# Kernel tuning notes

Measured on AMD Instinct MI355X. Metric: run time of the kernel, lower is better.

Reference implementation:

```python
import jax, jax.numpy as jnp
import numpy as np

D, K, HID, NBLK, N = 128, 256, 256, 2, 4096

def setup_inputs() -> dict:
    key = jax.random.key(0)
    ks = jax.random.split(key, 12)
    inp = {
        'x': jax.random.normal(ks[0], (N, D), jnp.float32),
        'x_hat': jax.random.normal(ks[1], (N, D), jnp.float32),
        'base_codebook': jax.random.normal(ks[2], (K, D), jnp.float32) * 0.1,
        # concat_proj: Linear(2D -> D), torch weight layout (out, in)
        'Wp': jax.random.normal(ks[3], (D, 2 * D), jnp.float32) / np.sqrt(2 * D),
        'bp': jnp.zeros((D,), jnp.float32),
        # residual blocks stacked over NBLK: Linear(D->HID), ReLU, Linear(HID->D)
        'W1': jax.random.normal(ks[4], (NBLK, HID, D), jnp.float32) / np.sqrt(D),
        'b1': jnp.zeros((NBLK, HID), jnp.float32),
        'W2': jax.random.normal(ks[5], (NBLK, D, HID), jnp.float32) / np.sqrt(HID),
        'b2': jnp.zeros((NBLK, D), jnp.float32),
    }
    return inp

def _forward(x, x_hat, base_codebook, Wp, bp, W1, b1, W2, b2):
    # concat_proj([x_hat, cbar]) decomposed: avoids materializing (N,K,2D)
    x_part = x_hat @ Wp[:, :D].T                      # (N, D)
    c_part = base_codebook @ Wp[:, D:].T + bp          # (K, D)
    C = x_part[:, None, :] + c_part[None, :, :]        # (N, K, D)
    for i in range(NBLK):
        h = jax.nn.relu(jnp.einsum('nkd,hd->nkh', C, W1[i]) + b1[i])
        C = C + jnp.einsum('nkh,dh->nkd', h, W2[i]) + b2[i]
    r = x - x_hat                                      # (N, D)
    dists = jnp.sum((r[:, None, :] - C) ** 2, axis=-1) # (N, K)
    codes = jnp.argmin(dists, axis=-1)                 # (N,)
    c_sel = jnp.take_along_axis(C, codes[:, None, None], axis=1)[:, 0, :]
    x_hat_new = x_hat + c_sel
    return codes, x_hat_new, r, c_sel

def reference(x, x_hat, base_codebook, Wp, bp, W1, b1, W2, b2):
    return _forward(x, x_hat, base_codebook, Wp, bp, W1, b1, W2, b2)
```

## Files before the change

kernel.cpp:

```cpp
#include <hip/hip_runtime.h>


#define QD    128
#define QK    256
#define QHID  256
#define QNBLK 2
#define QN    4096

typedef _Float16 f16;
typedef _Float16 f16x8  __attribute__((ext_vector_type(8)));
typedef float    f32x16 __attribute__((ext_vector_type(16)));
typedef unsigned u32x2  __attribute__((ext_vector_type(2)));

#define WS_CPART 0
#define WS_W1H   131072
#define WS_W1L   262144
#define WS_W2H   393216
#define WS_W2L   524288

#define L_WBUF  0
#define L_B1    65536
#define L_B2    67584
#define L_REDD  68608
#define L_REDI  69632
#define L_XP    70656
#define L_XH    71168
#define L_RS    71680
#define L_CSEL  72192
#define L_TOTAL 72704

static __device__ __forceinline__ f32x16 MF32(f16x8 a, f16x8 b, f32x16 c) {
    return __builtin_amdgcn_mfma_f32_32x32x16_f16(a, b, c, 0, 0, 0);
}
static __device__ __forceinline__ unsigned pkrtz(float a, float b) {
    return __builtin_bit_cast(unsigned, __builtin_amdgcn_cvt_pkrtz(a, b));
}
static __device__ __forceinline__ float f32lo(unsigned p) {
    return (float)__builtin_bit_cast(f16, (unsigned short)(p & 0xffffu));
}
static __device__ __forceinline__ float f32hi(unsigned p) {
    return (float)__builtin_bit_cast(f16, (unsigned short)(p >> 16));
}
static __device__ __forceinline__ u32x2 plswap(unsigned a, unsigned b) {
    return __builtin_amdgcn_permlane32_swap(a, b, false, false);
}
static __device__ __forceinline__ void gload_lds16(const void* g, void* l) {
    __builtin_amdgcn_global_load_lds(
        (const __attribute__((address_space(1))) unsigned*)g,
        (__attribute__((address_space(3))) unsigned*)l, 16, 0, 0);
}

template<int RB>
static __device__ __forceinline__ void split_frags(f32x16 a, f16x8& fh, f16x8& fl) {
    unsigned P0 = pkrtz(a[RB + 0], a[RB + 1]);
    unsigned P1 = pkrtz(a[RB + 2], a[RB + 3]);
    unsigned Q0 = pkrtz(a[RB + 4], a[RB + 5]);
    unsigned Q1 = pkrtz(a[RB + 6], a[RB + 7]);
    unsigned L0 = pkrtz(a[RB + 0] - f32lo(P0), a[RB + 1] - f32hi(P0));
    unsigned L1 = pkrtz(a[RB + 2] - f32lo(P1), a[RB + 3] - f32hi(P1));
    unsigned L2 = pkrtz(a[RB + 4] - f32lo(Q0), a[RB + 5] - f32hi(Q0));
    unsigned L3 = pkrtz(a[RB + 6] - f32lo(Q1), a[RB + 7] - f32hi(Q1));
    u32x2 s0 = plswap(P0, Q0);
    u32x2 s1 = plswap(P1, Q1);
    u32x2 t0 = plswap(L0, L2);
    u32x2 t1 = plswap(L1, L3);
    uint4 hw = make_uint4(s0.x, s1.x, s0.y, s1.y);
    uint4 lw = make_uint4(t0.x, t1.x, t0.y, t1.y);
    fh = __builtin_bit_cast(f16x8, hw);
    fl = __builtin_bit_cast(f16x8, lw);
}

__global__ __launch_bounds__(128) void qinco_prep(
    const float* __restrict__ cb, const float* __restrict__ Wp,
    const float* __restrict__ bp, const float* __restrict__ W1,
    const float* __restrict__ W2, char* __restrict__ ws) {
    const int blk = blockIdx.x;
    const int t = threadIdx.x;
    __shared__ float row[QD];

    if (blk < 256) {
        float* cpart = (float*)(ws + WS_CPART);
        row[t] = cb[blk * QD + t];
        __syncthreads();
        float acc = bp[t];
        const float* wr = Wp + (size_t)t * (2 * QD) + QD;
        #pragma unroll 8
        for (int e = 0; e < QD; ++e) acc = fmaf(row[e], wr[e], acc);
        cpart[blk * QD + t] = acc;
    } else if (blk < 384) {
        if (t < 64) {
            const int cid = blk - 256;
            const int b = cid >> 6, hc = (cid >> 3) & 7, kc = cid & 7;
            const int m = t & 31, g = t >> 5;
            f16* w1h = (f16*)(ws + WS_W1H);
            f16* w1l = (f16*)(ws + WS_W1L);
            #pragma unroll
            for (int j = 0; j < 8; ++j) {
                float wv = W1[((size_t)b * QHID + hc * 32 + m) * QD + kc * 16 + g * 8 + j];
                f16 hi = (f16)wv;
                size_t idx = ((size_t)cid * 64 + t) * 8 + j;
                w1h[idx] = hi;
                w1l[idx] = (f16)(wv - (float)hi);
            }
        }
    } else {
        if (t < 64) {
            const int e = blk - 384;
            const int b = e >> 6, hc = (e >> 3) & 7, dt = (e >> 1) & 3, kch = e & 1;
            const int m = t & 31, g = t >> 5;
            f16* w2h = (f16*)(ws + WS_W2H);
            f16* w2l = (f16*)(ws + WS_W2L);
            #pragma unroll
            for (int j = 0; j < 8; ++j) {
                float wv = W2[((size_t)b * QD + dt * 32 + m) * QHID + hc * 32 + kch * 16 + g * 8 + j];
                f16 hi = (f16)wv;
                size_t idx = ((size_t)e * 64 + t) * 8 + j;
                w2h[idx] = hi;
                w2l[idx] = (f16)(wv - (float)hi);
            }
        }
    }
}

__global__ __launch_bounds__(512, 2) void qinco_main(
    const float* __restrict__ x, const float* __restrict__ xh,
    const float* __restrict__ Wp,
    const float* __restrict__ b1g, const float* __restrict__ b2g,
    const char* __restrict__ ws, float* __restrict__ out) {

    extern __shared__ char smem[];
    const int n = blockIdx.x;
    const int t = threadIdx.x;
    const int w = t >> 6;
    const int l = t & 63;
    const int c32 = l & 31;
    const int g = l >> 5;
    const int baserow = w * 32;
    const int plane = w >> 1;
    const int jbase = (w & 1) * 4;

    float* b1_s  = (float*)(smem + L_B1);
    float* b2_s  = (float*)(smem + L_B2);
    float* red_d = (float*)(smem + L_REDD);
    int*   red_i = (int*)(smem + L_REDI);
    float* xp_s  = (float*)(smem + L_XP);
    float* xh_s  = (float*)(smem + L_XH);
    float* r_s   = (float*)(smem + L_RS);
    float* csel  = (float*)(smem + L_CSEL);

    const float* cpart = (const float*)(ws + WS_CPART);

    b1_s[t] = b1g[t];
    if (t < 2 * QD) b2_s[t] = b2g[t];
    if (t < QD) {
        float xv  = x[(size_t)n * QD + t];
        float xhv = xh[(size_t)n * QD + t];
        xh_s[t] = xhv;
        r_s[t]  = xv - xhv;
    }
    __syncthreads();

    if (t < QD) {
        const float4* wr = (const float4*)(Wp + (size_t)t * (2 * QD));
        const float4* xv = (const float4*)xh_s;
        float acc = 0.f;
        #pragma unroll
        for (int j = 0; j < QD / 4; ++j) {
            float4 a = wr[j], bv = xv[j];
            acc = fmaf(a.x, bv.x, acc);
            acc = fmaf(a.y, bv.y, acc);
            acc = fmaf(a.z, bv.z, acc);
            acc = fmaf(a.w, bv.w, acc);
        }
        xp_s[t] = acc;
    }
    __syncthreads();

    f32x16 Cacc[4];
    {
        const float* cprow = cpart + (size_t)(baserow + c32) * QD;
        #pragma unroll
        for (int dt = 0; dt < 4; ++dt)
            #pragma unroll
            for (int rq = 0; rq < 4; ++rq) {
                const int off = dt * 32 + 8 * rq + 4 * g;
                float4 cp  = *(const float4*)(cprow + off);
                float4 xp4 = *(const float4*)(xp_s + off);
                Cacc[dt][rq * 4 + 0] = cp.x + xp4.x;
                Cacc[dt][rq * 4 + 1] = cp.y + xp4.y;
                Cacc[dt][rq * 4 + 2] = cp.z + xp4.z;
                Cacc[dt][rq * 4 + 3] = cp.w + xp4.w;
            }
    }

    {
        const char* s0 = ws + (size_t)(plane + 1) * 131072 + (size_t)jbase * 1024
                       + (size_t)l * 16;
        char* d0 = smem + L_WBUF + (size_t)(plane * 8 + jbase) * 1024;
        #pragma unroll
        for (int ii = 0; ii < 4; ++ii)
            gload_lds16(s0 + (size_t)ii * 1024, d0 + (size_t)ii * 1024);
    }

    f16x8 cfh[8], cfl[8];

    #pragma unroll 1
    for (int iter = 0; iter < 16; ++iter) {
        const int cur = iter & 1;
        const int b = iter >> 3;
        const int hc = iter & 7;

        asm volatile("s_waitcnt vmcnt(0)" ::: "memory");
        __syncthreads();

        if (iter < 15) {
            const int it2 = iter + 1;
            const int bb = it2 >> 3, hh = it2 & 7;
            const char* s0 = ws + (size_t)(plane + 1) * 131072 + (size_t)bb * 65536
                           + (size_t)(hh * 8 + jbase) * 1024 + (size_t)l * 16;
            char* d0 = smem + L_WBUF + (size_t)(cur ^ 1) * 32768
                     + (size_t)(plane * 8 + jbase) * 1024;
            #pragma unroll
            for (int ii = 0; ii < 4; ++ii)
                gload_lds16(s0 + (size_t)ii * 1024, d0 + (size_t)ii * 1024);
        }

        if (hc == 0) {
            #pragma unroll
            for (int dt = 0; dt < 4; ++dt) {
                split_frags<0>(Cacc[dt], cfh[dt * 2 + 0], cfl[dt * 2 + 0]);
                split_frags<8>(Cacc[dt], cfh[dt * 2 + 1], cfl[dt * 2 + 1]);
            }
        }

        const char* wb = (const char*)smem + L_WBUF + (size_t)cur * 32768
                       + (size_t)l * 16;

        f32x16 Ha, Hb, Hc;
        #pragma unroll
        for (int rq = 0; rq < 4; ++rq) {
            float4 bv = *(const float4*)(b1_s + b * QHID + hc * 32 + 8 * rq + 4 * g);
            Ha[rq * 4 + 0] = bv.x;
            Ha[rq * 4 + 1] = bv.y;
            Ha[rq * 4 + 2] = bv.z;
            Ha[rq * 4 + 3] = bv.w;
        }
        #pragma unroll
        for (int r = 0; r < 16; ++r) { Hb[r] = 0.f; Hc[r] = 0.f; }

        __builtin_amdgcn_s_setprio(1);
        #pragma unroll
        for (int kc = 0; kc < 8; ++kc) {
            f16x8 wh = *(const f16x8*)(wb + kc * 1024);
            f16x8 wl = *(const f16x8*)(wb + 8192 + kc * 1024);
            Ha = MF32(wh, cfh[kc], Ha);
            Hb = MF32(wl, cfh[kc], Hb);
            Hc = MF32(wh, cfl[kc], Hc);
        }
        __builtin_amdgcn_s_setprio(0);

        f32x16 H;
        #pragma unroll
        for (int r = 0; r < 16; ++r)
            H[r] = fmaxf(Ha[r] + Hb[r] + Hc[r], 0.f);

        f16x8 hfh0, hfl0, hfh1, hfl1;
        split_frags<0>(H, hfh0, hfl0);
        split_frags<8>(H, hfh1, hfl1);

        __builtin_amdgcn_s_setprio(1);
        #pragma unroll
        for (int dt = 0; dt < 4; ++dt) {
            const char* q2h = wb + 16384 + (size_t)(dt * 2) * 1024;
            const char* q2l = wb + 24576 + (size_t)(dt * 2) * 1024;
            f16x8 w2h0 = *(const f16x8*)(q2h);
            f16x8 w2l0 = *(const f16x8*)(q2l);
            f16x8 w2h1 = *(const f16x8*)(q2h + 1024);
            f16x8 w2l1 = *(const f16x8*)(q2l + 1024);
            Cacc[dt] = MF32(w2h0, hfh0, Cacc[dt]);
            Cacc[dt] = MF32(w2l0, hfh0, Cacc[dt]);
            Cacc[dt] = MF32(w2h0, hfl0, Cacc[dt]);
            Cacc[dt] = MF32(w2h1, hfh1, Cacc[dt]);
            Cacc[dt] = MF32(w2l1, hfh1, Cacc[dt]);
            Cacc[dt] = MF32(w2h1, hfl1, Cacc[dt]);
        }
        __builtin_amdgcn_s_setprio(0);

        if (hc == 7) {
            #pragma unroll
            for (int dt = 0; dt < 4; ++dt)
                #pragma unroll
                for (int rq = 0; rq < 4; ++rq) {
                    float4 bv = *(const float4*)(b2_s + b * QD + dt * 32 + 8 * rq + 4 * g);
                    Cacc[dt][rq * 4 + 0] += bv.x;
                    Cacc[dt][rq * 4 + 1] += bv.y;
                    Cacc[dt][rq * 4 + 2] += bv.z;
                    Cacc[dt][rq * 4 + 3] += bv.w;
                }
        }
    }

    float pa = 0.f, pb = 0.f, pc = 0.f, pdm = 0.f;
    #pragma unroll
    for (int dt = 0; dt < 4; ++dt)
        #pragma unroll
        for (int rq = 0; rq < 4; ++rq) {
            float4 rr = *(const float4*)(r_s + dt * 32 + 8 * rq + 4 * g);
            float t0 = rr.x - Cacc[dt][rq * 4 + 0];
            float t1 = rr.y - Cacc[dt][rq * 4 + 1];
            float t2 = rr.z - Cacc[dt][rq * 4 + 2];
            float t3 = rr.w - Cacc[dt][rq * 4 + 3];
            pa = fmaf(t0, t0, pa);
            pb = fmaf(t1, t1, pb);
            pc = fmaf(t2, t2, pc);
            pdm = fmaf(t3, t3, pdm);
        }
    float pd = (pa + pb) + (pc + pdm);
    pd += __shfl_xor(pd, 32);
    if (l < 32) {
        red_d[baserow + l] = pd;
        red_i[baserow + l] = baserow + l;
    }
    __syncthreads();

    for (int off = 128; off > 0; off >>= 1) {
        if (t < off) {
            float d2 = red_d[t + off]; int i2 = red_i[t + off];
            float d1 = red_d[t];       int i1 = red_i[t];
            if (d2 < d1 || (d2 == d1 && i2 < i1)) { red_d[t] = d2; red_i[t] = i2; }
        }
        __syncthreads();
    }
    const int code = red_i[0];

    if (w == (code >> 5) && c32 == (code & 31)) {
        #pragma unroll
        for (int dt = 0; dt < 4; ++dt)
            #pragma unroll
            for (int rq = 0; rq < 4; ++rq)
                *(float4*)(csel + dt * 32 + 8 * rq + 4 * g) =
                    make_float4(Cacc[dt][rq * 4 + 0], Cacc[dt][rq * 4 + 1],
                                Cacc[dt][rq * 4 + 2], Cacc[dt][rq * 4 + 3]);
    }
    __syncthreads();

    if (t == 0) out[n] = (float)code;
    if (t < QD) {
        float cs  = csel[t];
        out[QN + (size_t)n * QD + t]                       = xh_s[t] + cs;
        out[QN + (size_t)QN * QD + (size_t)n * QD + t]     = r_s[t];
        out[QN + 2 * (size_t)QN * QD + (size_t)n * QD + t] = cs;
    }
}

extern "C" void kernel_launch(void* const* d_in, const int* in_sizes, int n_in,
                              void* d_out, int out_size, void* d_ws, size_t ws_size,
                              hipStream_t stream) {
    const float* x   = (const float*)d_in[0];
    const float* xh  = (const float*)d_in[1];
    const float* cb  = (const float*)d_in[2];
    const float* Wp  = (const float*)d_in[3];
    const float* bp  = (const float*)d_in[4];
    const float* W1  = (const float*)d_in[5];
    const float* b1  = (const float*)d_in[6];
    const float* W2  = (const float*)d_in[7];
    const float* b2  = (const float*)d_in[8];
    float* out = (float*)d_out;

    qinco_prep<<<512, 128, 0, stream>>>(cb, Wp, bp, W1, W2, (char*)d_ws);

    (void)hipFuncSetAttribute((const void*)qinco_main,
                              hipFuncAttributeMaxDynamicSharedMemorySize, L_TOTAL);
    qinco_main<<<QN, 512, L_TOTAL, stream>>>(x, xh, Wp, b1, b2,
                                             (const char*)d_ws, out);
}
```

Baseline: 716.0 us.

## Triple-buffer weight tiles in LDS with two-ahead prefetch and software-pipelined MFMA

```diff
diff --git a/kernel.cpp b/kernel.cpp
--- a/kernel.cpp
+++ b/kernel.cpp
@@ -19,15 +19,15 @@
 #define WS_W2L   524288
 
 #define L_WBUF  0
-#define L_B1    65536
-#define L_B2    67584
-#define L_REDD  68608
-#define L_REDI  69632
-#define L_XP    70656
-#define L_XH    71168
-#define L_RS    71680
-#define L_CSEL  72192
-#define L_TOTAL 72704
+#define L_B1    98304
+#define L_B2    100352
+#define L_REDD  101376
+#define L_REDI  102400
+#define L_XP    103424
+#define L_XH    103936
+#define L_RS    104448
+#define L_CSEL  104960
+#define L_TOTAL 105472
 
 static __device__ __forceinline__ f32x16 MF32(f16x8 a, f16x8 b, f32x16 c) {
     return __builtin_amdgcn_mfma_f32_32x32x16_f16(a, b, c, 0, 0, 0);
@@ -193,10 +193,12 @@
             }
     }
 
-    {
-        const char* s0 = ws + (size_t)(plane + 1) * 131072 + (size_t)jbase * 1024
-                       + (size_t)l * 16;
-        char* d0 = smem + L_WBUF + (size_t)(plane * 8 + jbase) * 1024;
+    #pragma unroll
+    for (int tt = 0; tt < 2; ++tt) {
+        const char* s0 = ws + (size_t)(plane + 1) * 131072
+                       + (size_t)(tt * 8 + jbase) * 1024 + (size_t)l * 16;
+        char* d0 = smem + L_WBUF + (size_t)tt * 32768
+                 + (size_t)(plane * 8 + jbase) * 1024;
         #pragma unroll
         for (int ii = 0; ii < 4; ++ii)
             gload_lds16(s0 + (size_t)ii * 1024, d0 + (size_t)ii * 1024);
@@ -206,24 +208,24 @@
 
     #pragma unroll 1
     for (int iter = 0; iter < 16; ++iter) {
-        const int cur = iter & 1;
+        if (iter < 15) asm volatile("s_waitcnt vmcnt(4)" ::: "memory");
+        else           asm volatile("s_waitcnt vmcnt(0)" ::: "memory");
+        __builtin_amdgcn_s_barrier();
+        asm volatile("" ::: "memory");
+
+        if (iter < 14) {
+            const int tt = iter + 2, bb = tt >> 3, hh = tt & 7;
+            const char* s0 = ws + (size_t)(plane + 1) * 131072 + (size_t)bb * 65536
+                           + (size_t)(hh * 8 + jbase) * 1024 + (size_t)l * 16;
+            char* d0 = smem + L_WBUF + (size_t)(tt % 3) * 32768
+                     + (size_t)(plane * 8 + jbase) * 1024;
+            #pragma unroll
+            for (int ii = 0; ii < 4; ++ii)
+                gload_lds16(s0 + (size_t)ii * 1024, d0 + (size_t)ii * 1024);
+        }
+
         const int b = iter >> 3;
         const int hc = iter & 7;
-
-        asm volatile("s_waitcnt vmcnt(0)" ::: "memory");
-        __syncthreads();
-
-        if (iter < 15) {
-            const int it2 = iter + 1;
-            const int bb = it2 >> 3, hh = it2 & 7;
-            const char* s0 = ws + (size_t)(plane + 1) * 131072 + (size_t)bb * 65536
-                           + (size_t)(hh * 8 + jbase) * 1024 + (size_t)l * 16;
-            char* d0 = smem + L_WBUF + (size_t)(cur ^ 1) * 32768
-                     + (size_t)(plane * 8 + jbase) * 1024;
-            #pragma unroll
-            for (int ii = 0; ii < 4; ++ii)
-                gload_lds16(s0 + (size_t)ii * 1024, d0 + (size_t)ii * 1024);
-        }
 
         if (hc == 0) {
             #pragma unroll
@@ -233,10 +235,10 @@
             }
         }
 
-        const char* wb = (const char*)smem + L_WBUF + (size_t)cur * 32768
+        const char* wb = (const char*)smem + L_WBUF + (size_t)(iter % 3) * 32768
                        + (size_t)l * 16;
 
-        f32x16 Ha, Hb, Hc;
+        f32x16 Ha;
         #pragma unroll
         for (int rq = 0; rq < 4; ++rq) {
             float4 bv = *(const float4*)(b1_s + b * QHID + hc * 32 + 8 * rq + 4 * g);
@@ -245,41 +247,50 @@
             Ha[rq * 4 + 2] = bv.z;
             Ha[rq * 4 + 3] = bv.w;
         }
-        #pragma unroll
-        for (int r = 0; r < 16; ++r) { Hb[r] = 0.f; Hc[r] = 0.f; }
-
+        f16x8 wh = *(const f16x8*)(wb);
+        f16x8 wl = *(const f16x8*)(wb + 8192);
         __builtin_amdgcn_s_setprio(1);
         #pragma unroll
         for (int kc = 0; kc < 8; ++kc) {
-            f16x8 wh = *(const f16x8*)(wb + kc * 1024);
-            f16x8 wl = *(const f16x8*)(wb + 8192 + kc * 1024);
+            f16x8 nh, nl;
+            if (kc < 7) {
+                nh = *(const f16x8*)(wb + (kc + 1) * 1024);
+                nl = *(const f16x8*)(wb + 8192 + (kc + 1) * 1024);
+            }
             Ha = MF32(wh, cfh[kc], Ha);
-            Hb = MF32(wl, cfh[kc], Hb);
-            Hc = MF32(wh, cfl[kc], Hc);
+            Ha = MF32(wl, cfh[kc], Ha);
+            Ha = MF32(wh, cfl[kc], Ha);
+            if (kc < 7) { wh = nh; wl = nl; }
         }
         __builtin_amdgcn_s_setprio(0);
 
-        f32x16 H;
-        #pragma unroll
-        for (int r = 0; r < 16; ++r)
-            H[r] = fmaxf(Ha[r] + Hb[r] + Hc[r], 0.f);
+        #pragma unroll
+        for (int r = 0; r < 16; ++r) Ha[r] = fmaxf(Ha[r], 0.f);
 
         f16x8 hfh0, hfl0, hfh1, hfl1;
-        split_frags<0>(H, hfh0, hfl0);
-        split_frags<8>(H, hfh1, hfl1);
+        split_frags<0>(Ha, hfh0, hfl0);
+
+        const char* q2h = wb + 16384;
+        const char* q2l = wb + 24576;
 
         __builtin_amdgcn_s_setprio(1);
         #pragma unroll
         for (int dt = 0; dt < 4; ++dt) {
-            const char* q2h = wb + 16384 + (size_t)(dt * 2) * 1024;
-            const char* q2l = wb + 24576 + (size_t)(dt * 2) * 1024;
-            f16x8 w2h0 = *(const f16x8*)(q2h);
-            f16x8 w2l0 = *(const f16x8*)(q2l);
-            f16x8 w2h1 = *(const f16x8*)(q2h + 1024);
-            f16x8 w2l1 = *(const f16x8*)(q2l + 1024);
+            f16x8 w2h0 = *(const f16x8*)(q2h + (size_t)(dt * 2) * 1024);
+            f16x8 w2l0 = *(const f16x8*)(q2l + (size_t)(dt * 2) * 1024);
             Cacc[dt] = MF32(w2h0, hfh0, Cacc[dt]);
             Cacc[dt] = MF32(w2l0, hfh0, Cacc[dt]);
             Cacc[dt] = MF32(w2h0, hfl0, Cacc[dt]);
+        }
+        __builtin_amdgcn_s_setprio(0);
+
+        split_frags<8>(Ha, hfh1, hfl1);
+
+        __builtin_amdgcn_s_setprio(1);
+        #pragma unroll
+        for (int dt = 0; dt < 4; ++dt) {
+            f16x8 w2h1 = *(const f16x8*)(q2h + (size_t)(dt * 2 + 1) * 1024);
+            f16x8 w2l1 = *(const f16x8*)(q2l + (size_t)(dt * 2 + 1) * 1024);
             Cacc[dt] = MF32(w2h1, hfh1, Cacc[dt]);
             Cacc[dt] = MF32(w2l1, hfh1, Cacc[dt]);
             Cacc[dt] = MF32(w2h1, hfl1, Cacc[dt]);
```

Measured after the change: 717.1 us. Within noise of the previous version (+0.1%).

## Split codes across four blocks per row with 16x16 MFMA and atomic argmin

Applied to the files above, without the earlier changes.

```diff
diff --git a/kernel.cpp b/kernel.cpp
--- a/kernel.cpp
+++ b/kernel.cpp
@@ -8,29 +8,17 @@
 #define QN    4096
 
 typedef _Float16 f16;
-typedef _Float16 f16x8  __attribute__((ext_vector_type(8)));
-typedef float    f32x16 __attribute__((ext_vector_type(16)));
-typedef unsigned u32x2  __attribute__((ext_vector_type(2)));
+typedef _Float16 f16x8 __attribute__((ext_vector_type(8)));
+typedef float    f32x4 __attribute__((ext_vector_type(4)));
+typedef unsigned long long u64;
 
 #define WS_CPART 0
-#define WS_W1H   131072
-#define WS_W1L   262144
-#define WS_W2H   393216
-#define WS_W2L   524288
-
-#define L_WBUF  0
-#define L_B1    65536
-#define L_B2    67584
-#define L_REDD  68608
-#define L_REDI  69632
-#define L_XP    70656
-#define L_XH    71168
-#define L_RS    71680
-#define L_CSEL  72192
-#define L_TOTAL 72704
-
-static __device__ __forceinline__ f32x16 MF32(f16x8 a, f16x8 b, f32x16 c) {
-    return __builtin_amdgcn_mfma_f32_32x32x16_f16(a, b, c, 0, 0, 0);
+#define WS_W1    131072
+#define WS_W2    393216
+#define WS_KEY   655360
+
+static __device__ __forceinline__ f32x4 MF16(f16x8 a, f16x8 b, f32x4 c) {
+    return __builtin_amdgcn_mfma_f32_16x16x32_f16(a, b, c, 0, 0, 0);
 }
 static __device__ __forceinline__ unsigned pkrtz(float a, float b) {
     return __builtin_bit_cast(unsigned, __builtin_amdgcn_cvt_pkrtz(a, b));
@@ -40,9 +28,6 @@
 }
 static __device__ __forceinline__ float f32hi(unsigned p) {
     return (float)__builtin_bit_cast(f16, (unsigned short)(p >> 16));
-}
-static __device__ __forceinline__ u32x2 plswap(unsigned a, unsigned b) {
-    return __builtin_amdgcn_permlane32_swap(a, b, false, false);
 }
 static __device__ __forceinline__ void gload_lds16(const void* g, void* l) {
     __builtin_amdgcn_global_load_lds(
@@ -50,24 +35,18 @@
         (__attribute__((address_space(3))) unsigned*)l, 16, 0, 0);
 }
 
-template<int RB>
-static __device__ __forceinline__ void split_frags(f32x16 a, f16x8& fh, f16x8& fl) {
-    unsigned P0 = pkrtz(a[RB + 0], a[RB + 1]);
-    unsigned P1 = pkrtz(a[RB + 2], a[RB + 3]);
-    unsigned Q0 = pkrtz(a[RB + 4], a[RB + 5]);
-    unsigned Q1 = pkrtz(a[RB + 6], a[RB + 7]);
-    unsigned L0 = pkrtz(a[RB + 0] - f32lo(P0), a[RB + 1] - f32hi(P0));
-    unsigned L1 = pkrtz(a[RB + 2] - f32lo(P1), a[RB + 3] - f32hi(P1));
-    unsigned L2 = pkrtz(a[RB + 4] - f32lo(Q0), a[RB + 5] - f32hi(Q0));
-    unsigned L3 = pkrtz(a[RB + 6] - f32lo(Q1), a[RB + 7] - f32hi(Q1));
-    u32x2 s0 = plswap(P0, Q0);
-    u32x2 s1 = plswap(P1, Q1);
-    u32x2 t0 = plswap(L0, L2);
-    u32x2 t1 = plswap(L1, L3);
-    uint4 hw = make_uint4(s0.x, s1.x, s0.y, s1.y);
-    uint4 lw = make_uint4(t0.x, t1.x, t0.y, t1.y);
-    fh = __builtin_bit_cast(f16x8, hw);
-    fl = __builtin_bit_cast(f16x8, lw);
+static __device__ __forceinline__ void mk_frag(f32x4 a0, f32x4 a1,
+                                               f16x8& fh, f16x8& fl) {
+    unsigned h0 = pkrtz(a0[0], a0[1]);
+    unsigned h1 = pkrtz(a0[2], a0[3]);
+    unsigned h2 = pkrtz(a1[0], a1[1]);
+    unsigned h3 = pkrtz(a1[2], a1[3]);
+    unsigned l0 = pkrtz(a0[0] - f32lo(h0), a0[1] - f32hi(h0));
+    unsigned l1 = pkrtz(a0[2] - f32lo(h1), a0[3] - f32hi(h1));
+    unsigned l2 = pkrtz(a1[0] - f32lo(h2), a1[1] - f32hi(h2));
+    unsigned l3 = pkrtz(a1[2] - f32lo(h3), a1[3] - f32hi(h3));
+    fh = __builtin_bit_cast(f16x8, make_uint4(h0, h1, h2, h3));
+    fl = __builtin_bit_cast(f16x8, make_uint4(l0, l1, l2, l3));
 }
 
 __global__ __launch_bounds__(128) void qinco_prep(
@@ -77,6 +56,9 @@
     const int blk = blockIdx.x;
     const int t = threadIdx.x;
     __shared__ float row[QD];
+
+    if (blk < 32)
+        ((u64*)(ws + WS_KEY))[blk * 128 + t] = ~0ull;
 
     if (blk < 256) {
         float* cpart = (float*)(ws + WS_CPART);
@@ -89,74 +71,82 @@
         cpart[blk * QD + t] = acc;
     } else if (blk < 384) {
         if (t < 64) {
-            const int cid = blk - 256;
-            const int b = cid >> 6, hc = (cid >> 3) & 7, kc = cid & 7;
-            const int m = t & 31, g = t >> 5;
-            f16* w1h = (f16*)(ws + WS_W1H);
-            f16* w1l = (f16*)(ws + WS_W1L);
+            const int u = blk - 256;
+            const int b = u >> 6, hc = (u >> 3) & 7, dc = (u >> 1) & 3, ht = u & 1;
+            const int lg = t >> 4;
+            const int h = hc * 32 + ht * 16 + (t & 15);
+            f16* dsth = (f16*)(ws + WS_W1
+                        + (size_t)(((b * 8 + hc) * 16 + dc * 4 + ht * 2) * 1024)
+                        + (size_t)t * 16);
+            f16* dstl = dsth + 512;
             #pragma unroll
             for (int j = 0; j < 8; ++j) {
-                float wv = W1[((size_t)b * QHID + hc * 32 + m) * QD + kc * 16 + g * 8 + j];
+                const int d = dc * 32 + 16 * (j >> 2) + 4 * lg + (j & 3);
+                float wv = W1[((size_t)b * QHID + h) * QD + d];
                 f16 hi = (f16)wv;
-                size_t idx = ((size_t)cid * 64 + t) * 8 + j;
-                w1h[idx] = hi;
-                w1l[idx] = (f16)(wv - (float)hi);
+                dsth[j] = hi;
+                dstl[j] = (f16)(wv - (float)hi);
             }
         }
     } else {
         if (t < 64) {
-            const int e = blk - 384;
-            const int b = e >> 6, hc = (e >> 3) & 7, dt = (e >> 1) & 3, kch = e & 1;
-            const int m = t & 31, g = t >> 5;
-            f16* w2h = (f16*)(ws + WS_W2H);
-            f16* w2l = (f16*)(ws + WS_W2L);
+            const int u = blk - 384;
+            const int b = u >> 6, hc = (u >> 3) & 7, dt = u & 7;
+            const int lg = t >> 4;
+            const int d = dt * 16 + (t & 15);
+            f16* dsth = (f16*)(ws + WS_W2
+                        + (size_t)(((b * 8 + hc) * 16 + dt * 2) * 1024)
+                        + (size_t)t * 16);
+            f16* dstl = dsth + 512;
             #pragma unroll
             for (int j = 0; j < 8; ++j) {
-                float wv = W2[((size_t)b * QD + dt * 32 + m) * QHID + hc * 32 + kch * 16 + g * 8 + j];
+                const int h = hc * 32 + 16 * (j >> 2) + 4 * lg + (j & 3);
+                float wv = W2[((size_t)b * QD + d) * QHID + h];
                 f16 hi = (f16)wv;
-                size_t idx = ((size_t)e * 64 + t) * 8 + j;
-                w2h[idx] = hi;
-                w2l[idx] = (f16)(wv - (float)hi);
+                dsth[j] = hi;
+                dstl[j] = (f16)(wv - (float)hi);
             }
         }
     }
 }
 
-__global__ __launch_bounds__(512, 2) void qinco_main(
+__global__ __launch_bounds__(256, 3) void qinco_main(
     const float* __restrict__ x, const float* __restrict__ xh,
     const float* __restrict__ Wp,
     const float* __restrict__ b1g, const float* __restrict__ b2g,
-    const char* __restrict__ ws, float* __restrict__ out) {
-
-    extern __shared__ char smem[];
-    const int n = blockIdx.x;
+    char* __restrict__ ws, float* __restrict__ out) {
+
+    __shared__ f16 wbuf[2][16][64][8];
+    __shared__ float b1_s[512];
+    __shared__ float b2_s[256];
+    __shared__ u64 red_k[64];
+    __shared__ float xp_s[QD], xh_s[QD], r_s[QD];
+
+    const int n = blockIdx.x >> 2;
+    const int h4 = blockIdx.x & 3;
     const int t = threadIdx.x;
     const int w = t >> 6;
     const int l = t & 63;
-    const int c32 = l & 31;
-    const int g = l >> 5;
-    const int baserow = w * 32;
-    const int plane = w >> 1;
-    const int jbase = (w & 1) * 4;
-
-    float* b1_s  = (float*)(smem + L_B1);
-    float* b2_s  = (float*)(smem + L_B2);
-    float* red_d = (float*)(smem + L_REDD);
-    int*   red_i = (int*)(smem + L_REDI);
-    float* xp_s  = (float*)(smem + L_XP);
-    float* xh_s  = (float*)(smem + L_XH);
-    float* r_s   = (float*)(smem + L_RS);
-    float* csel  = (float*)(smem + L_CSEL);
+    const int lg = l >> 4;
+    const int codebase = h4 * 64 + w * 16;
 
     const float* cpart = (const float*)(ws + WS_CPART);
 
     b1_s[t] = b1g[t];
-    if (t < 2 * QD) b2_s[t] = b2g[t];
+    b1_s[t + 256] = b1g[t + 256];
+    b2_s[t] = b2g[t];
     if (t < QD) {
         float xv  = x[(size_t)n * QD + t];
         float xhv = xh[(size_t)n * QD + t];
         xh_s[t] = xhv;
         r_s[t]  = xv - xhv;
+    }
+    {
+        const char* s0 = ws + WS_W1 + (size_t)(w * 4) * 1024 + (size_t)l * 16;
+        char* d0 = (char*)(&wbuf[0][w * 4][0][0]);
+        #pragma unroll
+        for (int ii = 0; ii < 4; ++ii)
+            gload_lds16(s0 + (size_t)ii * 1024, d0 + (size_t)ii * 1024);
     }
     __syncthreads();
 
@@ -176,50 +166,47 @@
     }
     __syncthreads();
 
-    f32x16 Cacc[4];
+    f32x4 Cacc[8];
     {
-        const float* cprow = cpart + (size_t)(baserow + c32) * QD;
-        #pragma unroll
-        for (int dt = 0; dt < 4; ++dt)
-            #pragma unroll
-            for (int rq = 0; rq < 4; ++rq) {
-                const int off = dt * 32 + 8 * rq + 4 * g;
-                float4 cp  = *(const float4*)(cprow + off);
-                float4 xp4 = *(const float4*)(xp_s + off);
-                Cacc[dt][rq * 4 + 0] = cp.x + xp4.x;
-                Cacc[dt][rq * 4 + 1] = cp.y + xp4.y;
-                Cacc[dt][rq * 4 + 2] = cp.z + xp4.z;
-                Cacc[dt][rq * 4 + 3] = cp.w + xp4.w;
-            }
-    }
-
-    {
-        const char* s0 = ws + (size_t)(plane + 1) * 131072 + (size_t)jbase * 1024
-                       + (size_t)l * 16;
-        char* d0 = smem + L_WBUF + (size_t)(plane * 8 + jbase) * 1024;
-        #pragma unroll
-        for (int ii = 0; ii < 4; ++ii)
-            gload_lds16(s0 + (size_t)ii * 1024, d0 + (size_t)ii * 1024);
-    }
-
-    f16x8 cfh[8], cfl[8];
+        const int code = codebase + (l & 15);
+        const float* cprow = cpart + (size_t)code * QD;
+        #pragma unroll
+        for (int dt = 0; dt < 8; ++dt) {
+            const int d0 = dt * 16 + 4 * lg;
+            float4 cp  = *(const float4*)(cprow + d0);
+            float4 xp4 = *(const float4*)(xp_s + d0);
+            Cacc[dt] = (f32x4){cp.x + xp4.x, cp.y + xp4.y,
+                               cp.z + xp4.z, cp.w + xp4.w};
+        }
+    }
+
+    f16x8 cfh[4], cfl[4];
 
     #pragma unroll 1
     for (int iter = 0; iter < 16; ++iter) {
-        const int cur = iter & 1;
         const int b = iter >> 3;
         const int hc = iter & 7;
-
-        asm volatile("s_waitcnt vmcnt(0)" ::: "memory");
-        __syncthreads();
+        const int buf = iter & 1;
+
+        asm volatile("s_waitcnt vmcnt(0) lgkmcnt(0)" ::: "memory");
+        __builtin_amdgcn_s_barrier();
+        asm volatile("" ::: "memory");
+
+        const char* pw2 = ws + WS_W2 + (size_t)((b * 8 + hc) * 16) * 1024
+                        + (size_t)l * 16;
+        f16x8 A0h[4], A0l[4];
+        #pragma unroll
+        for (int dt = 0; dt < 4; ++dt) {
+            A0h[dt] = *(const f16x8*)(pw2 + (size_t)(2 * dt) * 1024);
+            A0l[dt] = *(const f16x8*)(pw2 + (size_t)(2 * dt + 1) * 1024);
+        }
 
         if (iter < 15) {
-            const int it2 = iter + 1;
-            const int bb = it2 >> 3, hh = it2 & 7;
-            const char* s0 = ws + (size_t)(plane + 1) * 131072 + (size_t)bb * 65536
-                           + (size_t)(hh * 8 + jbase) * 1024 + (size_t)l * 16;
-            char* d0 = smem + L_WBUF + (size_t)(cur ^ 1) * 32768
-                     + (size_t)(plane * 8 + jbase) * 1024;
+            const int t2 = iter + 1;
+            const char* s0 = ws + WS_W1
+                           + (size_t)((((t2 >> 3) * 8 + (t2 & 7)) * 16 + w * 4)) * 1024
+                           + (size_t)l * 16;
+            char* d0 = (char*)(&wbuf[buf ^ 1][w * 4][0][0]);
             #pragma unroll
             for (int ii = 0; ii < 4; ++ii)
                 gload_lds16(s0 + (size_t)ii * 1024, d0 + (size_t)ii * 1024);
@@ -227,130 +214,212 @@
 
         if (hc == 0) {
             #pragma unroll
-            for (int dt = 0; dt < 4; ++dt) {
-                split_frags<0>(Cacc[dt], cfh[dt * 2 + 0], cfl[dt * 2 + 0]);
-                split_frags<8>(Cacc[dt], cfh[dt * 2 + 1], cfl[dt * 2 + 1]);
+            for (int c = 0; c < 4; ++c)
+                mk_frag(Cacc[2 * c], Cacc[2 * c + 1], cfh[c], cfl[c]);
+        }
+
+        f32x4 Ha0, Ha1;
+        {
+            float4 bv0 = *(const float4*)(b1_s + b * 256 + hc * 32 + 4 * lg);
+            float4 bv1 = *(const float4*)(b1_s + b * 256 + hc * 32 + 16 + 4 * lg);
+            Ha0 = (f32x4){bv0.x, bv0.y, bv0.z, bv0.w};
+            Ha1 = (f32x4){bv1.x, bv1.y, bv1.z, bv1.w};
+        }
+        const char* wb1 = (const char*)(&wbuf[buf][0][0][0]) + (size_t)l * 16;
+        __builtin_amdgcn_s_setprio(1);
+        #pragma unroll
+        for (int dc = 0; dc < 4; ++dc) {
+            f16x8 w1h0 = *(const f16x8*)(wb1 + (size_t)(dc * 4 + 0) * 1024);
+            f16x8 w1l0 = *(const f16x8*)(wb1 + (size_t)(dc * 4 + 1) * 1024);
+            f16x8 w1h1 = *(const f16x8*)(wb1 + (size_t)(dc * 4 + 2) * 1024);
+            f16x8 w1l1 = *(const f16x8*)(wb1 + (size_t)(dc * 4 + 3) * 1024);
+            Ha0 = MF16(w1h0, cfh[dc], Ha0);
+            Ha1 = MF16(w1h1, cfh[dc], Ha1);
+            Ha0 = MF16(w1l0, cfh[dc], Ha0);
+            Ha1 = MF16(w1l1, cfh[dc], Ha1);
+            Ha0 = MF16(w1h0, cfl[dc], Ha0);
+            Ha1 = MF16(w1h1, cfl[dc], Ha1);
+        }
+        __builtin_amdgcn_s_setprio(0);
+
+        #pragma unroll
+        for (int q = 0; q < 4; ++q) {
+            Ha0[q] = fmaxf(Ha0[q], 0.f);
+            Ha1[q] = fmaxf(Ha1[q], 0.f);
+        }
+        f16x8 hfh, hfl;
+        mk_frag(Ha0, Ha1, hfh, hfl);
+
+        __builtin_amdgcn_s_setprio(1);
+        #pragma unroll
+        for (int dt = 0; dt < 4; ++dt) {
+            Cacc[dt] = MF16(A0h[dt], hfh, Cacc[dt]);
+            Cacc[dt] = MF16(A0l[dt], hfh, Cacc[dt]);
+            Cacc[dt] = MF16(A0h[dt], hfl, Cacc[dt]);
+        }
+        __builtin_amdgcn_s_setprio(0);
+
+        f16x8 A1h[4], A1l[4];
+        #pragma unroll
+        for (int dt = 0; dt < 4; ++dt) {
+            A1h[dt] = *(const f16x8*)(pw2 + (size_t)(2 * (dt + 4)) * 1024);
+            A1l[dt] = *(const f16x8*)(pw2 + (size_t)(2 * (dt + 4) + 1) * 1024);
+        }
+        __builtin_amdgcn_s_setprio(1);
+        #pragma unroll
+        for (int dt = 0; dt < 4; ++dt) {
+            Cacc[dt + 4] = MF16(A1h[dt], hfh, Cacc[dt + 4]);
+            Cacc[dt + 4] = MF16(A1l[dt], hfh, Cacc[dt + 4]);
+            Cacc[dt + 4] = MF16(A1h[dt], hfl, Cacc[dt + 4]);
+        }
+        __builtin_amdgcn_s_setprio(0);
+
+        if (hc == 7) {
+            #pragma unroll
+            for (int dt = 0; dt < 8; ++dt) {
+                float4 bv = *(const float4*)(b2_s + b * QD + dt * 16 + 4 * lg);
+                Cacc[dt][0] += bv.x;
+                Cacc[dt][1] += bv.y;
+                Cacc[dt][2] += bv.z;
+                Cacc[dt][3] += bv.w;
             }
-        }
-
-        const char* wb = (const char*)smem + L_WBUF + (size_t)cur * 32768
-                       + (size_t)l * 16;
-
-        f32x16 Ha, Hb, Hc;
-        #pragma unroll
-        for (int rq = 0; rq < 4; ++rq) {
-            float4 bv = *(const float4*)(b1_s + b * QHID + hc * 32 + 8 * rq + 4 * g);
-            Ha[rq * 4 + 0] = bv.x;
-            Ha[rq * 4 + 1] = bv.y;
-            Ha[rq * 4 + 2] = bv.z;
-            Ha[rq * 4 + 3] = bv.w;
-        }
-        #pragma unroll
-        for (int r = 0; r < 16; ++r) { Hb[r] = 0.f; Hc[r] = 0.f; }
-
-        __builtin_amdgcn_s_setprio(1);
-        #pragma unroll
-        for (int kc = 0; kc < 8; ++kc) {
-            f16x8 wh = *(const f16x8*)(wb + kc * 1024);
-            f16x8 wl = *(const f16x8*)(wb + 8192 + kc * 1024);
-            Ha = MF32(wh, cfh[kc], Ha);
-            Hb = MF32(wl, cfh[kc], Hb);
-            Hc = MF32(wh, cfl[kc], Hc);
-        }
-        __builtin_amdgcn_s_setprio(0);
-
-        f32x16 H;
-        #pragma unroll
-        for (int r = 0; r < 16; ++r)
-            H[r] = fmaxf(Ha[r] + Hb[r] + Hc[r], 0.f);
-
-        f16x8 hfh0, hfl0, hfh1, hfl1;
-        split_frags<0>(H, hfh0, hfl0);
-        split_frags<8>(H, hfh1, hfl1);
-
-        __builtin_amdgcn_s_setprio(1);
-        #pragma unroll
-        for (int dt = 0; dt < 4; ++dt) {
-            const char* q2h = wb + 16384 + (size_t)(dt * 2) * 1024;
-            const char* q2l = wb + 24576 + (size_t)(dt * 2) * 1024;
-            f16x8 w2h0 = *(const f16x8*)(q2h);
-            f16x8 w2l0 = *(const f16x8*)(q2l);
-            f16x8 w2h1 = *(const f16x8*)(q2h + 1024);
-            f16x8 w2l1 = *(const f16x8*)(q2l + 1024);
-            Cacc[dt] = MF32(w2h0, hfh0, Cacc[dt]);
-            Cacc[dt] = MF32(w2l0, hfh0, Cacc[dt]);
-            Cacc[dt] = MF32(w2h0, hfl0, Cacc[dt]);
-            Cacc[dt] = MF32(w2h1, hfh1, Cacc[dt]);
-            Cacc[dt] = MF32(w2l1, hfh1, Cacc[dt]);
-            Cacc[dt] = MF32(w2h1, hfl1, Cacc[dt]);
-        }
-        __builtin_amdgcn_s_setprio(0);
-
-        if (hc == 7) {
-            #pragma unroll
-            for (int dt = 0; dt < 4; ++dt)
-                #pragma unroll
-                for (int rq = 0; rq < 4; ++rq) {
-                    float4 bv = *(const float4*)(b2_s + b * QD + dt * 32 + 8 * rq + 4 * g);
-                    Cacc[dt][rq * 4 + 0] += bv.x;
-                    Cacc[dt][rq * 4 + 1] += bv.y;
-                    Cacc[dt][rq * 4 + 2] += bv.z;
-                    Cacc[dt][rq * 4 + 3] += bv.w;
-                }
         }
     }
 
     float pa = 0.f, pb = 0.f, pc = 0.f, pdm = 0.f;
     #pragma unroll
-    for (int dt = 0; dt < 4; ++dt)
-        #pragma unroll
-        for (int rq = 0; rq < 4; ++rq) {
-            float4 rr = *(const float4*)(r_s + dt * 32 + 8 * rq + 4 * g);
-            float t0 = rr.x - Cacc[dt][rq * 4 + 0];
-            float t1 = rr.y - Cacc[dt][rq * 4 + 1];
-            float t2 = rr.z - Cacc[dt][rq * 4 + 2];
-            float t3 = rr.w - Cacc[dt][rq * 4 + 3];
-            pa = fmaf(t0, t0, pa);
-            pb = fmaf(t1, t1, pb);
-            pc = fmaf(t2, t2, pc);
-            pdm = fmaf(t3, t3, pdm);
-        }
+    for (int dt = 0; dt < 8; ++dt) {
+        float4 rr = *(const float4*)(r_s + dt * 16 + 4 * lg);
+        float t0 = rr.x - Cacc[dt][0];
+        float t1 = rr.y - Cacc[dt][1];
+        float t2 = rr.z - Cacc[dt][2];
+        float t3 = rr.w - Cacc[dt][3];
+        pa = fmaf(t0, t0, pa);
+        pb = fmaf(t1, t1, pb);
+        pc = fmaf(t2, t2, pc);
+        pdm = fmaf(t3, t3, pdm);
+    }
     float pd = (pa + pb) + (pc + pdm);
+    pd += __shfl_xor(pd, 16);
     pd += __shfl_xor(pd, 32);
-    if (l < 32) {
-        red_d[baserow + l] = pd;
-        red_i[baserow + l] = baserow + l;
+    if (l < 16) {
+        const int lc = w * 16 + l;
+        red_k[lc] = ((u64)__float_as_uint(pd) << 32)
+                  | (u64)(unsigned)(h4 * 64 + lc);
     }
     __syncthreads();
 
-    for (int off = 128; off > 0; off >>= 1) {
+    for (int off = 32; off > 0; off >>= 1) {
         if (t < off) {
-            float d2 = red_d[t + off]; int i2 = red_i[t + off];
-            float d1 = red_d[t];       int i1 = red_i[t];
-            if (d2 < d1 || (d2 == d1 && i2 < i1)) { red_d[t] = d2; red_i[t] = i2; }
+            u64 a = red_k[t], b2v = red_k[t + off];
+            red_k[t] = (b2v < a) ? b2v : a;
         }
         __syncthreads();
     }
-    const int code = red_i[0];
-
-    if (w == (code >> 5) && c32 == (code & 31)) {
-        #pragma unroll
-        for (int dt = 0; dt < 4; ++dt)
-            #pragma unroll
-            for (int rq = 0; rq < 4; ++rq)
-                *(float4*)(csel + dt * 32 + 8 * rq + 4 * g) =
-                    make_float4(Cacc[dt][rq * 4 + 0], Cacc[dt][rq * 4 + 1],
-                                Cacc[dt][rq * 4 + 2], Cacc[dt][rq * 4 + 3]);
-    }
+    if (t == 0)
+        atomicMin((u64*)(ws + WS_KEY) + n, red_k[0]);
+}
+
+__global__ __launch_bounds__(256) void qinco_fin(
+    const float* __restrict__ x, const float* __restrict__ xh,
+    const float* __restrict__ Wp,
+    const float* __restrict__ W1, const float* __restrict__ b1,
+    const float* __restrict__ W2, const float* __restrict__ b2,
+    const char* __restrict__ ws, float* __restrict__ out) {
+
+    __shared__ float xh4[4][QD];
+    __shared__ float C[4][QD];
+    __shared__ float s_l[QHID][4];
+    __shared__ int code_s[4];
+
+    const int t = threadIdx.x;
+    const int ng = blockIdx.x * 4;
+    const u64* keys = (const u64*)(ws + WS_KEY);
+    const float* cpart = (const float*)(ws + WS_CPART);
+
+    if (t < 4) code_s[t] = (int)(keys[ng + t] & 255u);
+    for (int i = t; i < 4 * QD; i += 256)
+        xh4[i >> 7][i & 127] = xh[(size_t)(ng + (i >> 7)) * QD + (i & 127)];
     __syncthreads();
 
-    if (t == 0) out[n] = (float)code;
-    if (t < QD) {
-        float cs  = csel[t];
-        out[QN + (size_t)n * QD + t]                       = xh_s[t] + cs;
-        out[QN + (size_t)QN * QD + (size_t)n * QD + t]     = r_s[t];
-        out[QN + 2 * (size_t)QN * QD + (size_t)n * QD + t] = cs;
-    }
+    const int d = t & 127, ph = t >> 7;
+
+    #pragma unroll
+    for (int k2 = 0; k2 < 2; ++k2) {
+        const int nl = ph + 2 * k2;
+        float acc = 0.f;
+        const float4* wr = (const float4*)(Wp + (size_t)d * (2 * QD));
+        #pragma unroll 8
+        for (int e4 = 0; e4 < 32; ++e4) {
+            float4 wv = wr[e4];
+            acc = fmaf(wv.x, xh4[nl][e4 * 4 + 0], acc);
+            acc = fmaf(wv.y, xh4[nl][e4 * 4 + 1], acc);
+            acc = fmaf(wv.z, xh4[nl][e4 * 4 + 2], acc);
+            acc = fmaf(wv.w, xh4[nl][e4 * 4 + 3], acc);
+        }
+        C[nl][d] = acc + cpart[(size_t)code_s[nl] * QD + d];
+    }
+    __syncthreads();
+
+    #pragma unroll 1
+    for (int b = 0; b < QNBLK; ++b) {
+        {
+            const int h = t;
+            float acc[4];
+            float bb = b1[b * QHID + h];
+            acc[0] = acc[1] = acc[2] = acc[3] = bb;
+            const float4* wr = (const float4*)(W1 + ((size_t)b * QHID + h) * QD);
+            #pragma unroll 4
+            for (int e4 = 0; e4 < 32; ++e4) {
+                float4 wv = wr[e4];
+                #pragma unroll
+                for (int nl = 0; nl < 4; ++nl) {
+                    acc[nl] = fmaf(wv.x, C[nl][e4 * 4 + 0], acc[nl]);
+                    acc[nl] = fmaf(wv.y, C[nl][e4 * 4 + 1], acc[nl]);
+                    acc[nl] = fmaf(wv.z, C[nl][e4 * 4 + 2], acc[nl]);
+                    acc[nl] = fmaf(wv.w, C[nl][e4 * 4 + 3], acc[nl]);
+                }
+            }
+            #pragma unroll
+            for (int nl = 0; nl < 4; ++nl)
+                s_l[h][nl] = fmaxf(acc[nl], 0.f);
+        }
+        __syncthreads();
+        {
+            float a0 = 0.f, a1 = 0.f;
+            const int nl0 = ph, nl1 = ph + 2;
+            const float4* wr = (const float4*)(W2 + ((size_t)b * QD + d) * QHID);
+            #pragma unroll 4
+            for (int h4i = 0; h4i < 64; ++h4i) {
+                float4 wv = wr[h4i];
+                a0 = fmaf(wv.x, s_l[h4i * 4 + 0][nl0], a0);
+                a1 = fmaf(wv.x, s_l[h4i * 4 + 0][nl1], a1);
+                a0 = fmaf(wv.y, s_l[h4i * 4 + 1][nl0], a0);
+                a1 = fmaf(wv.y, s_l[h4i * 4 + 1][nl1], a1);
+                a0 = fmaf(wv.z, s_l[h4i * 4 + 2][nl0], a0);
+                a1 = fmaf(wv.z, s_l[h4i * 4 + 2][nl1], a1);
+                a0 = fmaf(wv.w, s_l[h4i * 4 + 3][nl0], a0);
+                a1 = fmaf(wv.w, s_l[h4i * 4 + 3][nl1], a1);
+            }
+            float bv = b2[b * QD + d];
+            C[nl0][d] += a0 + bv;
+            C[nl1][d] += a1 + bv;
+        }
+        __syncthreads();
+    }
+
+    #pragma unroll
+    for (int k2 = 0; k2 < 2; ++k2) {
+        const int nl = ph + 2 * k2;
+        const size_t nn = (size_t)(ng + nl);
+        float cs = C[nl][d];
+        float xhv = xh4[nl][d];
+        float xv = x[nn * QD + d];
+        out[QN + nn * QD + d]                        = xhv + cs;
+        out[QN + (size_t)QN * QD + nn * QD + d]      = xv - xhv;
+        out[QN + 2 * (size_t)QN * QD + nn * QD + d]  = cs;
+    }
+    if (t < 4) out[ng + t] = (float)code_s[t];
 }
 
 extern "C" void kernel_launch(void* const* d_in, const int* in_sizes, int n_in,
@@ -368,9 +437,7 @@
     float* out = (float*)d_out;
 
     qinco_prep<<<512, 128, 0, stream>>>(cb, Wp, bp, W1, W2, (char*)d_ws);
-
-    (void)hipFuncSetAttribute((const void*)qinco_main,
-                              hipFuncAttributeMaxDynamicSharedMemorySize, L_TOTAL);
-    qinco_main<<<QN, 512, L_TOTAL, stream>>>(x, xh, Wp, b1, b2,
-                                             (const char*)d_ws, out);
-}
+    qinco_main<<<4 * QN, 256, 0, stream>>>(x, xh, Wp, b1, b2, (char*)d_ws, out);
+    qinco_fin<<<QN / 4, 256, 0, stream>>>(x, xh, Wp, W1, b1, W2, b2,
+                                          (const char*)d_ws, out);
+}
```

Result: slower. 972.7 us (+35.8%).
